# Kernel tuning notes

Measured on AMD Instinct MI355X. Metric: run time of the kernel, lower is better.

Reference implementation:

```python
import jax, jax.numpy as jnp
import numpy as np

N_NODES = 50000
N_EDGES = 800000
HIDDEN = 128


def setup_inputs() -> dict:
    key = jax.random.key(0)
    k_emb, k_ei, k1, k2, k3, kb1, kb2, kb3 = jax.random.split(key, 8)
    emb = jax.random.normal(k_emb, (N_NODES, HIDDEN), dtype=jnp.float32)
    edge_index = jax.random.randint(k_ei, (2, N_EDGES), 0, N_NODES, dtype=jnp.int64)
    h = HIDDEN
    # MLP([2h, 4h, h, 1]) weights, Kaiming-uniform-ish init
    def lin(k, fan_in, fan_out):
        bound = 1.0 / np.sqrt(fan_in)
        return jax.random.uniform(k, (fan_in, fan_out), jnp.float32, -bound, bound)
    W1 = lin(k1, 2 * h, 4 * h)
    b1 = jax.random.uniform(kb1, (4 * h,), jnp.float32, -1.0 / np.sqrt(2 * h), 1.0 / np.sqrt(2 * h))
    W2 = lin(k2, 4 * h, h)
    b2 = jax.random.uniform(kb2, (h,), jnp.float32, -1.0 / np.sqrt(4 * h), 1.0 / np.sqrt(4 * h))
    W3 = lin(k3, h, 1)
    b3 = jax.random.uniform(kb3, (1,), jnp.float32, -1.0 / np.sqrt(h), 1.0 / np.sqrt(h))
    return {"emb": emb, "edge_index": edge_index,
            "W1": W1, "b1": b1, "W2": W2, "b2": b2, "W3": W3, "b3": b3}


def reference(emb, edge_index, W1, b1, W2, b2, W3, b3):
    # learn_edge_att=True path: gather endpoints, concat, 3-layer MLP
    col, row = edge_index[0], edge_index[1]
    f12 = jnp.concatenate([emb[col], emb[row]], axis=-1)  # [E, 2h]
    x = jax.nn.relu(f12 @ W1 + b1)                         # [E, 4h]
    x = jax.nn.relu(x @ W2 + b2)                           # [E, h]
    att_log_logits = x @ W3 + b3                           # [E, 1]
    return att_log_logits
```

## Files before the change

kernel.cpp:

```cpp
#include <hip/hip_runtime.h>
#include <hip/hip_bf16.h>
#include <stdint.h>

#define N_EDGES   800000
#define N_NODESC  50000
#define HID       128

typedef __attribute__((ext_vector_type(8))) short bf16x8;
typedef __attribute__((ext_vector_type(4))) float f32x4;
typedef __attribute__((ext_vector_type(4))) unsigned int u32x4;

__device__ __forceinline__ short f2bf(float f) {
    union { float f; uint32_t u; } v; v.f = f;
    uint32_t r = v.u + 0x7FFFu + ((v.u >> 16) & 1u);
    return (short)(r >> 16);
}

__device__ __forceinline__ uint32_t packbf2(float lo, float hi) {
    float2 t; t.x = lo; t.y = hi;
    __hip_bfloat162 h = __float22bfloat162_rn(t);
    uint32_t u;
    __builtin_memcpy(&u, &h, 4);
    return u;
}

__device__ __forceinline__ uint32_t addrelu2(uint32_t a, uint32_t b) {
    __hip_bfloat162 ha, hb;
    __builtin_memcpy(&ha, &a, 4);
    __builtin_memcpy(&hb, &b, 4);
    __hip_bfloat162 s = __hadd2(ha, hb);
    uint32_t x;
    __builtin_memcpy(&x, &s, 4);
    uint32_t neg = (x & 0x80008000u) >> 15;
    return x & ~(neg * 0xFFFFu);
}
__device__ __forceinline__ bf16x8 addrelu8(u32x4 p, u32x4 q) {
    u32x4 r;
    #pragma unroll
    for (int j = 0; j < 4; ++j) r[j] = addrelu2(p[j], q[j]);
    bf16x8 out;
    __builtin_memcpy(&out, &r, 16);
    return out;
}

#define PQ_OFF    0UL
#define W1S_OFF   102400000UL
#define W2S_OFF   (W1S_OFF + 262144UL)
#define CNT_OFF   (W2S_OFF + 131072UL)
#define BSUM_OFF  (CNT_OFF + 200704UL)
#define CUR_OFF   (BSUM_OFF + 1024UL)
#define SPK_OFF   (CUR_OFF + 200704UL)
#define POS_OFF   (SPK_OFF + 3200000UL)
#define TMP_OFF   (POS_OFF + 3200000UL)

#define SCAN_BLOCKS 196

__global__ __launch_bounds__(256) void swizzle_kernel(const float* __restrict__ W1,
                                                      const float* __restrict__ W2,
                                                      short* __restrict__ W1s,
                                                      short* __restrict__ W2s) {
    int t = blockIdx.x * 256 + threadIdx.x;
    int lane = t & 63;
    int kq = lane >> 4;
    int nn = lane & 15;
    if (t < 16384) {
        int frag = t >> 6;
        int kc = frag >> 6;
        int nt = frag & 63;
        int n = nt * 16 + nn;
        int kbase = kc * 32 + kq * 8;
        bf16x8 v;
        #pragma unroll
        for (int j = 0; j < 8; ++j) {
            int k = kbase + j;
            float f = (n < 512) ? W1[k * 512 + n] : W1[(128 + k) * 512 + (n - 512)];
            v[j] = f2bf(f);
        }
        *(bf16x8*)(W1s + frag * 512 + lane * 8) = v;
    } else if (t < 24576) {
        int t2 = t - 16384;
        int frag = t2 >> 6;
        int kc = frag >> 3;
        int nt = frag & 7;
        int n = nt * 16 + nn;
        int kbase = kc * 32 + kq * 8;
        bf16x8 v;
        #pragma unroll
        for (int j = 0; j < 8; ++j) v[j] = f2bf(W2[(kbase + j) * HID + n]);
        *(bf16x8*)(W2s + frag * 512 + lane * 8) = v;
    }
}

__global__ __launch_bounds__(256) void precompute_kernel(const float* __restrict__ emb,
                                                         const short* __restrict__ W1s,
                                                         const float* __restrict__ b1,
                                                         short* __restrict__ PQ) {
    __shared__ short tile[4][16][272];
    int lane = threadIdx.x & 63;
    int w = threadIdx.x >> 6;
    int nb = blockIdx.x * 16;
    int m = lane & 15;
    int kq = lane >> 4;

    const float* arow = emb + (size_t)(nb + m) * 128 + kq * 8;

    f32x4 acc[16];
    #pragma unroll
    for (int i = 0; i < 16; ++i) acc[i] = (f32x4){0.f, 0.f, 0.f, 0.f};

    #pragma unroll
    for (int kc = 0; kc < 4; ++kc) {
        f32x4 x0 = *(const f32x4*)(arow + kc * 32);
        f32x4 x1 = *(const f32x4*)(arow + kc * 32 + 4);
        u32x4 au;
        au[0] = packbf2(x0[0], x0[1]); au[1] = packbf2(x0[2], x0[3]);
        au[2] = packbf2(x1[0], x1[1]); au[3] = packbf2(x1[2], x1[3]);
        bf16x8 a;
        __builtin_memcpy(&a, &au, 16);
        #pragma unroll
        for (int nt = 0; nt < 16; ++nt) {
            int frag = kc * 64 + (w * 16 + nt);
            bf16x8 b = *(const bf16x8*)(W1s + frag * 512 + lane * 8);
            acc[nt] = __builtin_amdgcn_mfma_f32_16x16x32_bf16(a, b, acc[nt], 0, 0, 0);
        }
    }

    #pragma unroll
    for (int nt = 0; nt < 16; ++nt) {
        int n = w * 256 + nt * 16 + m;
        float bias = (n < 512) ? b1[n] : 0.0f;
        #pragma unroll
        for (int r = 0; r < 4; ++r)
            tile[w][kq * 4 + r][nt * 16 + m] = f2bf(acc[nt][r] + bias);
    }

    #pragma unroll
    for (int s = 0; s < 8; ++s) {
        int row = s * 2 + (lane >> 5);
        int chunk = lane & 31;
        bf16x8 v = *(const bf16x8*)(&tile[w][row][chunk * 8]);
        *(bf16x8*)(PQ + (size_t)(nb + row) * 1024 + w * 256 + chunk * 8) = v;
    }
}


__global__ __launch_bounds__(256) void hist_kernel(const int* __restrict__ ei,
                                                   int* __restrict__ counts) {
    int e = blockIdx.x * 256 + threadIdx.x;
    atomicAdd(&counts[ei[e]], 1);
}

__global__ __launch_bounds__(256) void scan1_kernel(const int* __restrict__ counts,
                                                    int* __restrict__ cursor,
                                                    int* __restrict__ blocksum) {
    __shared__ int sm[256];
    int t = threadIdx.x;
    int i = blockIdx.x * 256 + t;
    int v = counts[i];
    sm[t] = v;
    __syncthreads();
    #pragma unroll
    for (int off = 1; off < 256; off <<= 1) {
        int y = (t >= off) ? sm[t - off] : 0;
        __syncthreads();
        sm[t] += y;
        __syncthreads();
    }
    cursor[i] = sm[t] - v;
    if (t == 255) blocksum[blockIdx.x] = sm[t];
}

__global__ __launch_bounds__(256) void finalize2_kernel(int* __restrict__ cursor,
                                                        const int* __restrict__ bsum) {
    __shared__ int wsum[4];
    int t = threadIdx.x;
    int b = blockIdx.x;
    int v = (t < b && t < SCAN_BLOCKS) ? bsum[t] : 0;
    #pragma unroll
    for (int off = 1; off < 64; off <<= 1) v += __shfl_xor(v, off, 64);
    if ((t & 63) == 0) wsum[t >> 6] = v;
    __syncthreads();
    int base = wsum[0] + wsum[1] + wsum[2] + wsum[3];
    cursor[b * 256 + t] += base;
}

__global__ __launch_bounds__(256) void scatter_kernel(const int* __restrict__ ei,
                                                      int* __restrict__ cursor,
                                                      unsigned int* __restrict__ spk,
                                                      int* __restrict__ pos) {
    int e = blockIdx.x * 256 + threadIdx.x;
    int c = ei[e];
    int r = ei[N_EDGES + e];
    int p = atomicAdd(&cursor[c], 1);
    spk[p] = ((unsigned int)r << 16) | (unsigned int)c;
    pos[e] = p;
}

__global__ __launch_bounds__(256, 3) void edge_kernel(const short* __restrict__ PQ,
                                                      const unsigned int* __restrict__ spk,
                                                      const short* __restrict__ W2s,
                                                      const float* __restrict__ b2,
                                                      const float* __restrict__ W3,
                                                      const float* __restrict__ b3,
                                                      float* __restrict__ tmp) {
    int lane = threadIdx.x & 63;
    int w = threadIdx.x >> 6;
    int e0 = blockIdx.x * 128 + w * 32;
    int m = lane & 15;
    int kq = lane >> 4;

    unsigned int pk = spk[e0 + (lane & 31)];

    const short* pb[2];
    const short* qb[2];
    #pragma unroll
    for (int t = 0; t < 2; ++t) {
        unsigned int v = __shfl(pk, t * 16 + m, 64);
        int ce = (int)(v & 0xFFFFu);
        int re = (int)(v >> 16);
        pb[t] = PQ + (size_t)ce * 1024 + kq * 8;
        qb[t] = PQ + (size_t)re * 1024 + 512 + kq * 8;
    }

    f32x4 acc[2][8];
    #pragma unroll
    for (int t = 0; t < 2; ++t)
        #pragma unroll
        for (int nt = 0; nt < 8; ++nt) acc[t][nt] = (f32x4){0.f, 0.f, 0.f, 0.f};

    #pragma unroll
    for (int kc = 0; kc < 16; ++kc) {
        u32x4 p[2], q[2];
        #pragma unroll
        for (int t = 0; t < 2; ++t) {
            p[t] = *(const u32x4*)(pb[t] + kc * 32);
            q[t] = *(const u32x4*)(qb[t] + kc * 32);
        }
        bf16x8 b[8];
        #pragma unroll
        for (int nt = 0; nt < 8; ++nt)
            b[nt] = *(const bf16x8*)(W2s + (kc * 8 + nt) * 512 + lane * 8);
        #pragma unroll
        for (int t = 0; t < 2; ++t) {
            bf16x8 a = addrelu8(p[t], q[t]);
            #pragma unroll
            for (int nt = 0; nt < 8; ++nt)
                acc[t][nt] = __builtin_amdgcn_mfma_f32_16x16x32_bf16(a, b[nt], acc[t][nt], 0, 0, 0);
        }
    }

    float b2v[8], w3v[8];
    #pragma unroll
    for (int nt = 0; nt < 8; ++nt) {
        b2v[nt] = b2[nt * 16 + m];
        w3v[nt] = W3[nt * 16 + m];
    }
    float b3s = b3[0];
    #pragma unroll
    for (int t = 0; t < 2; ++t) {
        float partial[4] = {0.f, 0.f, 0.f, 0.f};
        #pragma unroll
        for (int nt = 0; nt < 8; ++nt) {
            #pragma unroll
            for (int r = 0; r < 4; ++r) {
                float x2 = acc[t][nt][r] + b2v[nt];
                x2 = x2 > 0.f ? x2 : 0.f;
                partial[r] += x2 * w3v[nt];
            }
        }
        #pragma unroll
        for (int r = 0; r < 4; ++r) {
            #pragma unroll
            for (int off = 1; off < 16; off <<= 1)
                partial[r] += __shfl_xor(partial[r], off, 64);
        }
        if (m == 0) {
            f32x4 v;
            #pragma unroll
            for (int r = 0; r < 4; ++r) v[r] = partial[r] + b3s;
            *(f32x4*)(tmp + e0 + t * 16 + kq * 4) = v;
        }
    }
}

__global__ __launch_bounds__(256) void permute_kernel(const float* __restrict__ tmp,
                                                      const int* __restrict__ pos,
                                                      float* __restrict__ out) {
    int e = blockIdx.x * 256 + threadIdx.x;
    out[e] = tmp[pos[e]];
}

extern "C" void kernel_launch(void* const* d_in, const int* in_sizes, int n_in,
                              void* d_out, int out_size, void* d_ws, size_t ws_size,
                              hipStream_t stream) {
    const float* emb = (const float*)d_in[0];
    const int*   ei  = (const int*)d_in[1];
    const float* W1  = (const float*)d_in[2];
    const float* b1  = (const float*)d_in[3];
    const float* W2  = (const float*)d_in[4];
    const float* b2  = (const float*)d_in[5];
    const float* W3  = (const float*)d_in[6];
    const float* b3  = (const float*)d_in[7];
    float* out = (float*)d_out;

    short* PQ   = (short*)((char*)d_ws + PQ_OFF);
    short* W1s  = (short*)((char*)d_ws + W1S_OFF);
    short* W2s  = (short*)((char*)d_ws + W2S_OFF);
    int* counts = (int*)((char*)d_ws + CNT_OFF);
    int* bsum   = (int*)((char*)d_ws + BSUM_OFF);
    int* cursor = (int*)((char*)d_ws + CUR_OFF);
    unsigned int* spk = (unsigned int*)((char*)d_ws + SPK_OFF);
    int* pos    = (int*)((char*)d_ws + POS_OFF);
    float* tmp  = (float*)((char*)d_ws + TMP_OFF);

    swizzle_kernel<<<96, 256, 0, stream>>>(W1, W2, W1s, W2s);
    hipMemsetAsync(counts, 0, SCAN_BLOCKS * 256 * sizeof(int), stream);
    hist_kernel<<<N_EDGES / 256, 256, 0, stream>>>(ei, counts);
    scan1_kernel<<<SCAN_BLOCKS, 256, 0, stream>>>(counts, cursor, bsum);
    finalize2_kernel<<<SCAN_BLOCKS, 256, 0, stream>>>(cursor, bsum);
    scatter_kernel<<<N_EDGES / 256, 256, 0, stream>>>(ei, cursor, spk, pos);

    precompute_kernel<<<N_NODESC / 16, 256, 0, stream>>>(emb, W1s, b1, PQ);
    edge_kernel<<<N_EDGES / 128, 256, 0, stream>>>(PQ, spk, W2s, b2, W3, b3, tmp);
    permute_kernel<<<N_EDGES / 256, 256, 0, stream>>>(tmp, pos, out);
}
```

Measured before the change: 455.6 us.

## Split edge histogram into eight segments to cut atomic contention in counting sort

The counting sort over source nodes now keeps eight separate histograms, chosen by block index modulo eight, so histogram and scatter atomics spread across more addresses. The prefix scan becomes a three-pass scan over the segment-major counts array, and the scanned counts serve directly as scatter cursors. This aims to reduce atomic contention in hist and scatter. In exchange, the memset and scan cover eight times more data and add a single-block scan pass and an extra kernel launch. It also changes the order of edges within each node group, which can affect edge-kernel locality.

```diff
diff --git a/kernel.cpp b/kernel.cpp
--- a/kernel.cpp
+++ b/kernel.cpp
@@ -47,13 +47,15 @@
 #define W1S_OFF   102400000UL
 #define W2S_OFF   (W1S_OFF + 262144UL)
 #define CNT_OFF   (W2S_OFF + 131072UL)
-#define BSUM_OFF  (CNT_OFF + 200704UL)
-#define CUR_OFF   (BSUM_OFF + 1024UL)
-#define SPK_OFF   (CUR_OFF + 200704UL)
+#define BSUM_OFF  (CNT_OFF + 1605632UL)
+#define SPK_OFF   (BSUM_OFF + 8192UL)
 #define POS_OFF   (SPK_OFF + 3200000UL)
 #define TMP_OFF   (POS_OFF + 3200000UL)
 
-#define SCAN_BLOCKS 196
+#define NBINS     50176
+#define NSEG      8
+#define SCAN_N    (NSEG * NBINS)
+#define SCANA_BLOCKS 1568
 
 __global__ __launch_bounds__(256) void swizzle_kernel(const float* __restrict__ W1,
                                                       const float* __restrict__ W2,
@@ -147,12 +149,12 @@
 __global__ __launch_bounds__(256) void hist_kernel(const int* __restrict__ ei,
                                                    int* __restrict__ counts) {
     int e = blockIdx.x * 256 + threadIdx.x;
-    atomicAdd(&counts[ei[e]], 1);
-}
-
-__global__ __launch_bounds__(256) void scan1_kernel(const int* __restrict__ counts,
-                                                    int* __restrict__ cursor,
-                                                    int* __restrict__ blocksum) {
+    int seg = blockIdx.x & 7;
+    atomicAdd(&counts[seg * NBINS + ei[e]], 1);
+}
+
+__global__ __launch_bounds__(256) void scanA_kernel(int* __restrict__ counts,
+                                                    int* __restrict__ bsum) {
     __shared__ int sm[256];
     int t = threadIdx.x;
     int i = blockIdx.x * 256 + t;
@@ -166,22 +168,43 @@
         sm[t] += y;
         __syncthreads();
     }
-    cursor[i] = sm[t] - v;
-    if (t == 255) blocksum[blockIdx.x] = sm[t];
-}
-
-__global__ __launch_bounds__(256) void finalize2_kernel(int* __restrict__ cursor,
-                                                        const int* __restrict__ bsum) {
-    __shared__ int wsum[4];
+    counts[i] = sm[t] - v;
+    if (t == 255) bsum[blockIdx.x] = sm[t];
+}
+
+__global__ __launch_bounds__(256) void scanB_kernel(int* __restrict__ bsum) {
+    __shared__ int sm[256];
     int t = threadIdx.x;
-    int b = blockIdx.x;
-    int v = (t < b && t < SCAN_BLOCKS) ? bsum[t] : 0;
-    #pragma unroll
-    for (int off = 1; off < 64; off <<= 1) v += __shfl_xor(v, off, 64);
-    if ((t & 63) == 0) wsum[t >> 6] = v;
+    int local = 0;
+    #pragma unroll
+    for (int j = 0; j < 7; ++j) {
+        int idx = t * 7 + j;
+        local += (idx < SCANA_BLOCKS) ? bsum[idx] : 0;
+    }
+    sm[t] = local;
     __syncthreads();
-    int base = wsum[0] + wsum[1] + wsum[2] + wsum[3];
-    cursor[b * 256 + t] += base;
+    #pragma unroll
+    for (int off = 1; off < 256; off <<= 1) {
+        int y = (t >= off) ? sm[t - off] : 0;
+        __syncthreads();
+        sm[t] += y;
+        __syncthreads();
+    }
+    int running = sm[t] - local;
+    #pragma unroll
+    for (int j = 0; j < 7; ++j) {
+        int idx = t * 7 + j;
+        if (idx < SCANA_BLOCKS) {
+            int c = bsum[idx];
+            bsum[idx] = running;
+            running += c;
+        }
+    }
+}
+
+__global__ __launch_bounds__(256) void scanC_kernel(int* __restrict__ counts,
+                                                    const int* __restrict__ bsum) {
+    counts[blockIdx.x * 256 + threadIdx.x] += bsum[blockIdx.x];
 }
 
 __global__ __launch_bounds__(256) void scatter_kernel(const int* __restrict__ ei,
@@ -189,9 +212,10 @@
                                                       unsigned int* __restrict__ spk,
                                                       int* __restrict__ pos) {
     int e = blockIdx.x * 256 + threadIdx.x;
+    int seg = blockIdx.x & 7;
     int c = ei[e];
     int r = ei[N_EDGES + e];
-    int p = atomicAdd(&cursor[c], 1);
+    int p = atomicAdd(&cursor[seg * NBINS + c], 1);
     spk[p] = ((unsigned int)r << 16) | (unsigned int)c;
     pos[e] = p;
 }
@@ -308,17 +332,17 @@
     short* W2s  = (short*)((char*)d_ws + W2S_OFF);
     int* counts = (int*)((char*)d_ws + CNT_OFF);
     int* bsum   = (int*)((char*)d_ws + BSUM_OFF);
-    int* cursor = (int*)((char*)d_ws + CUR_OFF);
     unsigned int* spk = (unsigned int*)((char*)d_ws + SPK_OFF);
     int* pos    = (int*)((char*)d_ws + POS_OFF);
     float* tmp  = (float*)((char*)d_ws + TMP_OFF);
 
     swizzle_kernel<<<96, 256, 0, stream>>>(W1, W2, W1s, W2s);
-    hipMemsetAsync(counts, 0, SCAN_BLOCKS * 256 * sizeof(int), stream);
+    hipMemsetAsync(counts, 0, SCAN_N * sizeof(int), stream);
     hist_kernel<<<N_EDGES / 256, 256, 0, stream>>>(ei, counts);
-    scan1_kernel<<<SCAN_BLOCKS, 256, 0, stream>>>(counts, cursor, bsum);
-    finalize2_kernel<<<SCAN_BLOCKS, 256, 0, stream>>>(cursor, bsum);
-    scatter_kernel<<<N_EDGES / 256, 256, 0, stream>>>(ei, cursor, spk, pos);
+    scanA_kernel<<<SCANA_BLOCKS, 256, 0, stream>>>(counts, bsum);
+    scanB_kernel<<<1, 256, 0, stream>>>(bsum);
+    scanC_kernel<<<SCANA_BLOCKS, 256, 0, stream>>>(counts, bsum);
+    scatter_kernel<<<N_EDGES / 256, 256, 0, stream>>>(ei, counts, spk, pos);
 
     precompute_kernel<<<N_NODESC / 16, 256, 0, stream>>>(emb, W1s, b1, PQ);
     edge_kernel<<<N_EDGES / 128, 256, 0, stream>>>(PQ, spk, W2s, b2, W3, b3, tmp);
```

After: 457.6 us. Within noise of the previous version (+0.4%).

## Split edge histogram into 8 segmented counters to cut atomic contention

Applied to the files above, without the earlier changes.

Replaces the single per-node histogram and cursor with 8 segment-private copies, selected by block index, for the counting sort of edges by source node. The scan runs over the interleaved (node, segment) space, so each segment gets a contiguous slot range inside each node's bucket, and scatter then uses the segment-local cursor. This is meant to spread atomics over more addresses. In exchange it adds an 8x larger memset, a larger scan, and a finalize whose per-block prefix loop over up to 1568 block sums grows with block index.

```diff
diff --git a/kernel.cpp b/kernel.cpp
--- a/kernel.cpp
+++ b/kernel.cpp
@@ -47,13 +47,15 @@
 #define W1S_OFF   102400000UL
 #define W2S_OFF   (W1S_OFF + 262144UL)
 #define CNT_OFF   (W2S_OFF + 131072UL)
-#define BSUM_OFF  (CNT_OFF + 200704UL)
-#define CUR_OFF   (BSUM_OFF + 1024UL)
-#define SPK_OFF   (CUR_OFF + 200704UL)
+#define BSUM_OFF  (CNT_OFF + 1605632UL)
+#define SPK_OFF   (BSUM_OFF + 8192UL)
 #define POS_OFF   (SPK_OFF + 3200000UL)
 #define TMP_OFF   (POS_OFF + 3200000UL)
 
-#define SCAN_BLOCKS 196
+#define NBINS     50176
+#define NSEG      8
+#define SCAN_N    (NSEG * NBINS)
+#define SCANA_BLOCKS 1568
 
 __global__ __launch_bounds__(256) void swizzle_kernel(const float* __restrict__ W1,
                                                       const float* __restrict__ W2,
@@ -147,16 +149,17 @@
 __global__ __launch_bounds__(256) void hist_kernel(const int* __restrict__ ei,
                                                    int* __restrict__ counts) {
     int e = blockIdx.x * 256 + threadIdx.x;
-    atomicAdd(&counts[ei[e]], 1);
-}
-
-__global__ __launch_bounds__(256) void scan1_kernel(const int* __restrict__ counts,
-                                                    int* __restrict__ cursor,
-                                                    int* __restrict__ blocksum) {
+    int seg = blockIdx.x & 7;
+    atomicAdd(&counts[seg * NBINS + ei[e]], 1);
+}
+
+__global__ __launch_bounds__(256) void scanA_kernel(int* __restrict__ counts,
+                                                    int* __restrict__ bsum) {
     __shared__ int sm[256];
     int t = threadIdx.x;
-    int i = blockIdx.x * 256 + t;
-    int v = counts[i];
+    int e = blockIdx.x * 256 + t;
+    int addr = (e & 7) * NBINS + (e >> 3);
+    int v = counts[addr];
     sm[t] = v;
     __syncthreads();
     #pragma unroll
@@ -166,22 +169,24 @@
         sm[t] += y;
         __syncthreads();
     }
-    cursor[i] = sm[t] - v;
-    if (t == 255) blocksum[blockIdx.x] = sm[t];
-}
-
-__global__ __launch_bounds__(256) void finalize2_kernel(int* __restrict__ cursor,
+    counts[addr] = sm[t] - v;
+    if (t == 255) bsum[blockIdx.x] = sm[t];
+}
+
+__global__ __launch_bounds__(256) void finalizeC_kernel(int* __restrict__ counts,
                                                         const int* __restrict__ bsum) {
     __shared__ int wsum[4];
     int t = threadIdx.x;
     int b = blockIdx.x;
-    int v = (t < b && t < SCAN_BLOCKS) ? bsum[t] : 0;
+    int v = 0;
+    for (int idx = t; idx < b; idx += 256) v += bsum[idx];
     #pragma unroll
     for (int off = 1; off < 64; off <<= 1) v += __shfl_xor(v, off, 64);
     if ((t & 63) == 0) wsum[t >> 6] = v;
     __syncthreads();
     int base = wsum[0] + wsum[1] + wsum[2] + wsum[3];
-    cursor[b * 256 + t] += base;
+    int e = b * 256 + t;
+    counts[(e & 7) * NBINS + (e >> 3)] += base;
 }
 
 __global__ __launch_bounds__(256) void scatter_kernel(const int* __restrict__ ei,
@@ -189,9 +194,10 @@
                                                       unsigned int* __restrict__ spk,
                                                       int* __restrict__ pos) {
     int e = blockIdx.x * 256 + threadIdx.x;
+    int seg = blockIdx.x & 7;
     int c = ei[e];
     int r = ei[N_EDGES + e];
-    int p = atomicAdd(&cursor[c], 1);
+    int p = atomicAdd(&cursor[seg * NBINS + c], 1);
     spk[p] = ((unsigned int)r << 16) | (unsigned int)c;
     pos[e] = p;
 }
@@ -308,17 +314,16 @@
     short* W2s  = (short*)((char*)d_ws + W2S_OFF);
     int* counts = (int*)((char*)d_ws + CNT_OFF);
     int* bsum   = (int*)((char*)d_ws + BSUM_OFF);
-    int* cursor = (int*)((char*)d_ws + CUR_OFF);
     unsigned int* spk = (unsigned int*)((char*)d_ws + SPK_OFF);
     int* pos    = (int*)((char*)d_ws + POS_OFF);
     float* tmp  = (float*)((char*)d_ws + TMP_OFF);
 
     swizzle_kernel<<<96, 256, 0, stream>>>(W1, W2, W1s, W2s);
-    hipMemsetAsync(counts, 0, SCAN_BLOCKS * 256 * sizeof(int), stream);
+    hipMemsetAsync(counts, 0, SCAN_N * sizeof(int), stream);
     hist_kernel<<<N_EDGES / 256, 256, 0, stream>>>(ei, counts);
-    scan1_kernel<<<SCAN_BLOCKS, 256, 0, stream>>>(counts, cursor, bsum);
-    finalize2_kernel<<<SCAN_BLOCKS, 256, 0, stream>>>(cursor, bsum);
-    scatter_kernel<<<N_EDGES / 256, 256, 0, stream>>>(ei, cursor, spk, pos);
+    scanA_kernel<<<SCANA_BLOCKS, 256, 0, stream>>>(counts, bsum);
+    finalizeC_kernel<<<SCANA_BLOCKS, 256, 0, stream>>>(counts, bsum);
+    scatter_kernel<<<N_EDGES / 256, 256, 0, stream>>>(ei, counts, spk, pos);
 
     precompute_kernel<<<N_NODESC / 16, 256, 0, stream>>>(emb, W1s, b1, PQ);
     edge_kernel<<<N_EDGES / 128, 256, 0, stream>>>(PQ, spk, W2s, b2, W3, b3, tmp);
```

After: 452.9 us. About the same (-0.6%).
